# Kernel tuning notes

Measured on AMD Instinct MI355X. Metric: run time of the kernel, lower is better.

## Reference

```python
import jax, jax.numpy as jnp
import numpy as np

V, E, H, C = 100000, 300, 512, 3
SP, SH, B = 64, 32, 128


def lstm_scan(x, Wih, Whh, b):
    # x: [T, B, E]; PyTorch gate order i, f, g, o
    T, Bb, _ = x.shape
    Hh = Whh.shape[1]
    h0 = jnp.zeros((Bb, Hh), x.dtype)

    def step(carry, xt):
        h, c = carry
        g = xt @ Wih.T + h @ Whh.T + b
        i, f, gg, o = jnp.split(g, 4, axis=-1)
        c = jax.nn.sigmoid(f) * c + jax.nn.sigmoid(i) * jnp.tanh(gg)
        h = jax.nn.sigmoid(o) * jnp.tanh(c)
        return (h, c), h

    _, hs = jax.lax.scan(step, (h0, h0), x)
    return hs  # [T, B, H]


def setup_inputs() -> dict:
    key = jax.random.key(0)
    ks = jax.random.split(key, 20)
    inv_sqrt_h = 1.0 / np.sqrt(H).astype(np.float32)

    def u(k, shape, scale):
        return (jax.random.uniform(k, shape, jnp.float32) * 2.0 - 1.0) * scale

    embed_table = jax.random.normal(ks[4], (V, E), jnp.float32) * 0.1
    embed_table = embed_table.at[0].set(0.0)  # padding_idx=0
    return {
        "premise": jax.random.randint(ks[0], (SP, B), 1, V),
        "premise_len": jax.random.randint(ks[1], (B,), 1, SP + 1),
        "hypothesis": jax.random.randint(ks[2], (SH, B), 1, V),
        "hypothesis_len": jax.random.randint(ks[3], (B,), 1, SH + 1),
        "embed_table": embed_table,
        "p_Wih": u(ks[5], (4 * H, E), inv_sqrt_h),
        "p_Whh": u(ks[6], (4 * H, H), inv_sqrt_h),
        "p_b": u(ks[7], (4 * H,), inv_sqrt_h),
        "h_Wih": u(ks[8], (4 * H, E), inv_sqrt_h),
        "h_Whh": u(ks[9], (4 * H, H), inv_sqrt_h),
        "h_b": u(ks[10], (4 * H,), inv_sqrt_h),
        "m_Wih": u(ks[11], (4 * H, 2 * H), inv_sqrt_h),
        "m_Whh": u(ks[12], (4 * H, H), inv_sqrt_h),
        "m_b": u(ks[13], (4 * H,), inv_sqrt_h),
        "w_e": jax.random.uniform(ks[14], (H,), jnp.float32),
        "Ws": u(ks[15], (H, H), np.sqrt(6.0 / (2 * H)).astype(np.float32)),
        "Wt": u(ks[16], (H, H), np.sqrt(6.0 / (2 * H)).astype(np.float32)),
        "Wm": u(ks[17], (H, H), np.sqrt(6.0 / (2 * H)).astype(np.float32)),
        "fc_W": u(ks[18], (C, H), np.sqrt(6.0 / (H + C)).astype(np.float32)),
        "fc_b": jnp.zeros((C,), jnp.float32),
    }


def reference(premise, premise_len, hypothesis, hypothesis_len, embed_table,
              p_Wih, p_Whh, p_b, h_Wih, h_Whh, h_b, m_Wih, m_Whh, m_b,
              w_e, Ws, Wt, Wm, fc_W, fc_b):
    Sp, Bb = premise.shape
    Sh = hypothesis.shape[0]
    Hh = Ws.shape[0]

    # Encoder LSTMs; emulate pack/pad: outputs past length are zeros
    h_s = lstm_scan(embed_table[premise], p_Wih, p_Whh, p_b)  # [Sp,B,H]
    h_s = h_s * (jnp.arange(Sp)[:, None] < premise_len[None, :]).astype(h_s.dtype)[:, :, None]
    h_t = lstm_scan(embed_table[hypothesis], h_Wih, h_Whh, h_b)  # [Sh,B,H]
    h_t = h_t * (jnp.arange(Sh)[:, None] < hypothesis_len[None, :]).astype(h_t.dtype)[:, :, None]

    Ws_hs = jnp.einsum('sbe,he->sbh', h_s, Ws)  # precompute premise projection

    def step(carry, inputs):
        h_m, c_m, h_last = carry
        h_t_k, k = inputs
        q = h_t_k @ Wt.T + h_m @ Wm.T                              # [B,H]
        e = jnp.einsum('sbh,h->sb', jnp.tanh(Ws_hs + q[None]), w_e)  # [Sp,B]
        alpha = jax.nn.softmax(e, axis=0)                           # softmax over premise (no mask, as in original)
        a_k = jnp.einsum('sb,sbh->bh', alpha, h_s)
        m_k = jnp.concatenate([a_k, h_t_k], axis=1)                 # [B,2H]
        g = m_k @ m_Wih.T + h_m @ m_Whh.T + m_b
        i, f, gg, o = jnp.split(g, 4, axis=-1)
        c_new = jax.nn.sigmoid(f) * c_m + jax.nn.sigmoid(i) * jnp.tanh(gg)
        h_new = jax.nn.sigmoid(o) * jnp.tanh(c_new)
        h_last = jnp.where((k + 1 == hypothesis_len)[:, None], h_new, h_last)
        return (h_new, c_new, h_last), None

    z = jnp.zeros((Bb, Hh), h_s.dtype)
    (_, _, h_last), _ = jax.lax.scan(step, (z, z, z), (h_t, jnp.arange(Sh)))
    return h_last @ fc_W.T + fc_b  # [B, C]
```

## Files before the change

### kernel.cpp

```cpp
#include <hip/hip_runtime.h>


#define NWG 256
#define TPB 512

typedef float f8v __attribute__((ext_vector_type(8)));

#define O_XPP      0ull
#define O_HTMW     0ull
#define O_HTWT     8388608ull
#define O_WSHS     10485760ull
#define O_XPH      16777216ull
#define O_HST      25165824ull
#define O_HS2      29360128ull
#define O_HTT      33554432ull
#define O_WIHTP    35651584ull
#define O_WIHTH    36265984ull
#define O_WHHPP    36880384ull
#define O_WHHPH    37928960ull
#define O_DW       38977536ull
#define O_WST      41074688ull
#define O_WTT      41336832ull
#define O_MWIHRT   41598976ull
#define O_BPP      42647552ull
#define O_BPH      42649600ull
#define O_BPM      42651648ull
#define O_HT2      42653696ull
#define O_HMT2     42784768ull
#define O_QBUF     42915840ull
#define O_AK2      42981376ull
#define O_HLAST    43046912ull
#define WS_FLOATS  43112448ull

__device__ unsigned g_cnt = 0u;
__device__ unsigned g_gen = 0u;
__device__ unsigned g_FE[NWG * 16];
__device__ unsigned g_FA[NWG * 16];
__device__ unsigned g_FB[NWG * 16];
__device__ unsigned g_FD[NWG * 16];
__device__ unsigned g_base2 = 0u;

struct Params {
  const int* premise; const int* plen; const int* hyp; const int* hlen;
  const float* embed;
  const float* pWih; const float* pWhh; const float* pb;
  const float* hWih; const float* hWhh; const float* hb;
  const float* mWih; const float* mWhh; const float* mb;
  const float* we; const float* Ws; const float* Wt; const float* Wm;
  const float* fcW; const float* fcb;
  float* out; float* ws;
};

__device__ __forceinline__ float2 sysld2(const float* p){
  unsigned long long u = __hip_atomic_load((const unsigned long long*)p,
      __ATOMIC_RELAXED, __HIP_MEMORY_SCOPE_SYSTEM);
  union { unsigned long long u; float2 f; } c; c.u = u; return c.f;
}
__device__ __forceinline__ void sysst(float* p, float v){
  union { float f; unsigned u; } c; c.f = v;
  __hip_atomic_store((unsigned*)p, c.u, __ATOMIC_RELAXED, __HIP_MEMORY_SCOPE_SYSTEM);
}
__device__ __forceinline__ void fbump(unsigned* a, unsigned v){
  __hip_atomic_store(a, v, __ATOMIC_RELAXED, __HIP_MEMORY_SCOPE_SYSTEM);
}
__device__ __forceinline__ void waitflag(const unsigned* a, unsigned tgt){
  while ((int)(__hip_atomic_load(a, __ATOMIC_RELAXED,
               __HIP_MEMORY_SCOPE_SYSTEM) - tgt) < 0)
    __builtin_amdgcn_s_sleep(1);
}

__device__ __forceinline__ void gbarH(){
  __syncthreads();
  if (threadIdx.x == 0){
    __threadfence();
    unsigned snap = __hip_atomic_load(&g_gen, __ATOMIC_RELAXED, __HIP_MEMORY_SCOPE_AGENT);
    unsigned n = __hip_atomic_fetch_add(&g_cnt, 1u, __ATOMIC_ACQ_REL, __HIP_MEMORY_SCOPE_AGENT);
    if ((n & 255u) == 255u){
      __hip_atomic_store(&g_gen, snap + 1u, __ATOMIC_RELEASE, __HIP_MEMORY_SCOPE_AGENT);
    } else {
      unsigned g;
      do {
        __builtin_amdgcn_s_sleep(2);
        g = __hip_atomic_load(&g_gen, __ATOMIC_ACQUIRE, __HIP_MEMORY_SCOPE_AGENT);
      } while ((int)(g - snap) <= 0);
    }
  }
  __syncthreads();
}

__device__ __forceinline__ float sigf(float x){ return 1.0f/(1.0f + __expf(-x)); }
__device__ __forceinline__ float tanhf_(float x){ return 2.0f/(1.0f + __expf(-2.0f*x)) - 1.0f; }

__device__ __forceinline__ float wsum(float v){
  #pragma unroll
  for (int o = 32; o > 0; o >>= 1) v += __shfl_xor(v, o, 64);
  return v;
}
__device__ __forceinline__ float wmaxr(float v){
  #pragma unroll
  for (int o = 32; o > 0; o >>= 1) v = fmaxf(v, __shfl_xor(v, o, 64));
  return v;
}

__device__ void lstm_enc(int wg, int tid, int lane, int cg, int bg, int T,
    const float* __restrict__ XP, const float* __restrict__ WPair,
    const int* __restrict__ lens, float* hbuf,
    float* __restrict__ houtT, float* __restrict__ hout2, float* lds,
    unsigned tb)
{
  const int b8 = tid & 7, hc32 = (tid >> 3) & 31, gp = tid >> 8;
  const int b = bg*8 + b8, hc = cg*32 + hc32;
  const float* wrow = WPair + (size_t)(hc*2 + gp) * 1024;
  const int mylen = lens[b];
  const int sb = tid >> 6, sk = (tid & 63) * 8;
  float* stage = lds;
  float* xch   = lds + 8*516;
  float c_reg = 0.f;
  const unsigned* peer = &g_FE[(((unsigned)bg << 4) | (lane & 15)) * 16];

  for (int t = 0; t < T; ++t){
    const float* hin  = hbuf + (size_t)(t & 1) * 65536;
    float*       hout = hbuf + (size_t)((t + 1) & 1) * 65536;
    if (lane < 16) waitflag(peer, tb + t);
    if (t > 0){
      const float* src = hin + (size_t)(bg*8 + sb)*512 + sk;
      float2 v0 = sysld2(src), v1 = sysld2(src+2), v2 = sysld2(src+4), v3 = sysld2(src+6);
      float* dst = stage + sb*516 + sk;
      float4 w0 = {v0.x, v0.y, v1.x, v1.y};
      float4 w1 = {v2.x, v2.y, v3.x, v3.y};
      *(float4*)dst = w0; *(float4*)(dst+4) = w1;
    }
    __syncthreads();
    float a0 = 0.f, a1 = 0.f;
    if (t > 0){
      const float* hr = stage + b8*516;
      #pragma unroll 2
      for (int k = 0; k < 512; k += 4){
        float4 h4 = *(const float4*)(hr + k);
        float4 wA = *(const float4*)(wrow + k*2);
        float4 wB = *(const float4*)(wrow + k*2 + 4);
        a0 += h4.x*wA.x + h4.y*wA.z + h4.z*wB.x + h4.w*wB.z;
        a1 += h4.x*wA.y + h4.y*wA.w + h4.z*wB.y + h4.w*wB.w;
      }
    }
    float2 xg = *(const float2*)(XP + ((size_t)t*128 + b)*2048 + hc*4 + gp*2);
    a0 += xg.x; a1 += xg.y;
    if (gp == 1){ xch[(b8*32+hc32)*2+0] = a0; xch[(b8*32+hc32)*2+1] = a1; }
    __syncthreads();
    if (gp == 0){
      float gg = xch[(b8*32+hc32)*2+0], go = xch[(b8*32+hc32)*2+1];
      float iv = sigf(a0), fv = sigf(a1), gv = tanhf_(gg), ov = sigf(go);
      c_reg = fv * c_reg + iv * gv;
      float hv = ov * tanhf_(c_reg);
      sysst(hout + (size_t)b*512 + hc, hv);
      float hm = (t < mylen) ? hv : 0.f;
      houtT[((size_t)t*512 + hc)*128 + b] = hm;
      if (hout2) hout2[((size_t)t*128 + b)*512 + hc] = hm;
    }
    __syncthreads();
    if (tid == 0) fbump(&g_FE[wg*16], tb + t + 1);
  }
}

__global__ __launch_bounds__(TPB, 2) void mlstm(Params p){
  const int wg = blockIdx.x, tid = threadIdx.x;
  const int lane = tid & 63, wave = tid >> 6;
  const int gtid = wg * TPB + tid;
  const int gwave = wg * 8 + wave;
  const int cg = wg & 15, bg = wg >> 4;
  __shared__ float lds[8736];
  __shared__ unsigned sh_base;

  if (tid == 0)
    sh_base = __hip_atomic_load(&g_base2, __ATOMIC_RELAXED, __HIP_MEMORY_SCOPE_SYSTEM);
  __syncthreads();
  const unsigned B = sh_base;

  float* const ws     = p.ws;
  float* const XPp    = ws + O_XPP;
  float* const XPh    = ws + O_XPH;
  float* const htmW   = ws + O_HTMW;
  float* const htWt   = ws + O_HTWT;
  float* const Ws_hs  = ws + O_WSHS;
  float* const h_sT   = ws + O_HST;
  float* const h_s2   = ws + O_HS2;
  float* const h_tT   = ws + O_HTT;
  float* const WihTp  = ws + O_WIHTP;
  float* const WihTh  = ws + O_WIHTH;
  float* const WhhPP  = ws + O_WHHPP;
  float* const WhhPH  = ws + O_WHHPH;
  float* const DW     = ws + O_DW;
  float* const WsT    = ws + O_WST;
  float* const WtT    = ws + O_WTT;
  float* const mWihRT = ws + O_MWIHRT;
  float* const bpP    = ws + O_BPP;
  float* const bpH    = ws + O_BPH;
  float* const bpM    = ws + O_BPM;
  float* const hT2    = ws + O_HT2;
  float* const hmT2   = ws + O_HMT2;
  float* const qbuf   = ws + O_QBUF;
  float* const ak2    = ws + O_AK2;
  float* const hlast  = ws + O_HLAST;

  for (int idx = gtid; idx < 300*2048; idx += NWG*TPB){
    int e = idx >> 11, jp = idx & 2047;
    int oc = (jp & 3) * 512 + (jp >> 2);
    WihTp[idx] = p.pWih[(size_t)oc*300 + e];
    WihTh[idx] = p.hWih[(size_t)oc*300 + e];
  }
  for (int idx = gtid; idx < 1024*512*2; idx += NWG*TPB){
    int g = idx & 1, k = (idx >> 1) & 511, pp = idx >> 10;
    int hc = pp >> 1, gp = pp & 1, oc = (gp*2+g)*512 + hc;
    WhhPP[idx] = p.pWhh[(size_t)oc*512 + k];
    WhhPH[idx] = p.hWhh[(size_t)oc*512 + k];
  }
  for (int idx = gtid; idx < 1024*1024*2; idx += NWG*TPB){
    int g = idx & 1, k = (idx >> 1) & 1023, pp = idx >> 11;
    int hc = pp >> 1, gp = pp & 1, oc = (gp*2+g)*512 + hc;
    DW[idx] = (k < 512) ? p.mWih[(size_t)oc*1024 + k]
                        : p.mWhh[(size_t)oc*512 + (k - 512)];
  }
  for (int idx = gtid; idx < 512*512; idx += NWG*TPB){
    int k = idx >> 9, h = idx & 511;
    WsT[idx] = p.Ws[(size_t)h*512 + k];
    WtT[idx] = p.Wt[(size_t)h*512 + k];
  }
  for (int idx = gtid; idx < 512*2048; idx += NWG*TPB){
    int k = idx >> 11, jp = idx & 2047;
    int oc = (jp & 3) * 512 + (jp >> 2);
    mWihRT[idx] = p.mWih[(size_t)oc*1024 + 512 + k];
  }
  for (int idx = gtid; idx < 2048; idx += NWG*TPB){
    int oc = (idx & 3) * 512 + (idx >> 2);
    bpP[idx] = p.pb[oc]; bpH[idx] = p.hb[oc]; bpM[idx] = p.mb[oc];
  }
  gbarH();

  for (int task = gwave; task < 6144; task += NWG*8){
    const bool prem = task < 4096;
    int rb, cb;
    if (prem){ cb = task >> 10; rb = task & 1023; }
    else { int t2 = task - 4096; cb = t2 >> 9; rb = t2 & 511; }
    const int r0 = rb * 8;
    const int* toks = prem ? p.premise : p.hyp;
    const float* wT = prem ? WihTp : WihTh;
    const float* bias = prem ? bpP : bpH;
    float* outp = prem ? XPp : XPh;
    const int j0 = cb * 512 + lane * 8;
    const float* xr[8];
    #pragma unroll
    for (int r = 0; r < 8; ++r) xr[r] = p.embed + (size_t)toks[r0 + r] * 300;
    f8v bias8 = *(const f8v*)(bias + j0);
    float acc[8][8];
    #pragma unroll
    for (int r = 0; r < 8; ++r){
      #pragma unroll
      for (int i = 0; i < 8; ++i) acc[r][i] = 0.f;
    }
    for (int e = 0; e < 300; ++e){
      f8v w8 = *(const f8v*)(wT + (size_t)e * 2048 + j0);
      #pragma unroll
      for (int r = 0; r < 8; ++r){
        float xv = xr[r][e];
        #pragma unroll
        for (int i = 0; i < 8; ++i) acc[r][i] += xv * w8[i];
      }
    }
    #pragma unroll
    for (int r = 0; r < 8; ++r){
      f8v o8;
      #pragma unroll
      for (int i = 0; i < 8; ++i) o8[i] = acc[r][i] + bias8[i];
      *(f8v*)(outp + (size_t)(r0 + r) * 2048 + j0) = o8;
    }
  }
  gbarH();

  lstm_enc(wg, tid, lane, cg, bg, 64, XPp, WhhPP, p.plen, hT2, h_sT, h_s2, lds, B);
  lstm_enc(wg, tid, lane, cg, bg, 32, XPh, WhhPH, p.hlen, hT2, h_tT, nullptr, lds, B + 64);
  gbarH();

  for (int task = gwave; task < 3584; task += NWG*8){
    const float* src; const float* wT; const float* bias; float* outp;
    int rb, cb, cols;
    if (task < 1024){ rb = task;        cb = 0;            src = h_sT; wT = WsT;    bias = nullptr; outp = Ws_hs; cols = 512; }
    else if (task < 1536){ rb = task-1024; cb = 0;         src = h_tT; wT = WtT;    bias = nullptr; outp = htWt;  cols = 512; }
    else { int t2 = task - 1536; cb = t2 >> 9; rb = t2 & 511; src = h_tT; wT = mWihRT; bias = bpM;  outp = htmW;  cols = 2048; }
    const int r0 = rb * 8;
    const int j0 = cb * 512 + lane * 8;
    const float* xr[8];
    #pragma unroll
    for (int r = 0; r < 8; ++r){
      int row = r0 + r;
      xr[r] = src + (size_t)(row >> 7) * 65536 + (row & 127);
    }
    f8v bias8 = {0,0,0,0,0,0,0,0};
    if (bias) bias8 = *(const f8v*)(bias + j0);
    float acc[8][8];
    #pragma unroll
    for (int r = 0; r < 8; ++r){
      #pragma unroll
      for (int i = 0; i < 8; ++i) acc[r][i] = 0.f;
    }
    for (int k = 0; k < 512; ++k){
      f8v w8 = *(const f8v*)(wT + (size_t)k * cols + j0);
      #pragma unroll
      for (int r = 0; r < 8; ++r){
        float xv = xr[r][(size_t)k * 128];
        #pragma unroll
        for (int i = 0; i < 8; ++i) acc[r][i] += xv * w8[i];
      }
    }
    #pragma unroll
    for (int r = 0; r < 8; ++r){
      f8v o8;
      #pragma unroll
      for (int i = 0; i < 8; ++i) o8[i] = acc[r][i] + bias8[i];
      *(f8v*)(outp + (size_t)(r0 + r) * (size_t)cols + j0) = o8;
    }
  }
  gbarH();

  const int b8 = tid & 7, hc32 = (tid >> 3) & 31, gp = tid >> 8;
  const int mb_ = bg*8 + b8, mhc = cg*32 + hc32;
  const float* dwrow = DW + (size_t)(mhc*2 + gp) * 2048;
  const int hyplen_b = p.hlen[mb_];
  const int sb = tid >> 6, sk = (tid & 63) * 8;
  float* stage  = lds;
  float* xchA   = lds + 8*516;
  float* stage2 = lds;
  float* xch2   = lds + 8*1028;
  float cm_reg = 0.f, hl_reg = 0.f;
  const unsigned* peerFD = &g_FD[(((unsigned)bg << 4) | (lane & 15)) * 16];
  const unsigned* rowFB  = &g_FB[((unsigned)(bg*8) + (lane & 7)) * 16];

  for (int k = 0; k < 32; ++k){
    const float* hmin  = hmT2 + (size_t)(k & 1) * 65536;
    float*       hmout = hmT2 + (size_t)((k + 1) & 1) * 65536;

    if (lane < 16) waitflag(peerFD, B + k);
    else if (lane < 24) waitflag(&g_FB[((unsigned)(bg*8) + (lane - 16)) * 16], B + k);
    if (k > 0){
      const float* src = hmin + (size_t)(bg*8 + sb)*512 + sk;
      float2 v0 = sysld2(src), v1 = sysld2(src+2), v2 = sysld2(src+4), v3 = sysld2(src+6);
      float* dst = stage + sb*516 + sk;
      float4 w0 = {v0.x, v0.y, v1.x, v1.y};
      float4 w1 = {v2.x, v2.y, v3.x, v3.y};
      *(float4*)dst = w0; *(float4*)(dst+4) = w1;
    }
    __syncthreads();
    {
      const int c32 = (tid >> 3) & 31, half = tid >> 8;
      const int c = cg*32 + c32;
      float a = 0.f;
      if (k > 0){
        const float* hr = stage + b8*516 + half*256;
        const float* wr = p.Wm + (size_t)c*512 + half*256;
        #pragma unroll 2
        for (int kk = 0; kk < 256; kk += 4){
          float4 h4 = *(const float4*)(hr + kk);
          float4 w4 = *(const float4*)(wr + kk);
          a += h4.x*w4.x + h4.y*w4.y + h4.z*w4.z + h4.w*w4.w;
        }
      }
      if (half == 1) xchA[c32*8 + b8] = a;
      __syncthreads();
      if (half == 0){
        float v = a + xchA[c32*8 + b8] + htWt[((size_t)k*128 + mb_)*512 + c];
        sysst(qbuf + (size_t)mb_*512 + c, v);
      }
    }
    __syncthreads();
    if (tid == 0) fbump(&g_FA[wg*16], B + k + 1);

    if (wg < 128){
      const int bb = wg;
      if (lane < 16) waitflag(&g_FA[(((unsigned)(bb >> 3) << 4) | lane) * 16], B + k + 1);
      else if (lane < 32) waitflag(&g_FD[(((unsigned)(bb >> 3) << 4) | (lane - 16)) * 16], B + k);
      const float* qb = qbuf + (size_t)bb*512 + lane*8;
      float2 qa = sysld2(qb), qbv = sysld2(qb+2), qc = sysld2(qb+4), qd = sysld2(qb+6);
      float4 q0 = {qa.x, qa.y, qbv.x, qbv.y};
      float4 q1 = {qc.x, qc.y, qd.x, qd.y};
      float4 e0 = *(const float4*)(p.we + lane*8);
      float4 e1 = *(const float4*)(p.we + lane*8 + 4);
      #pragma unroll
      for (int si = 0; si < 8; ++si){
        int s = wave*8 + si;
        const float* wsr = Ws_hs + ((size_t)s*128 + bb)*512 + lane*8;
        float4 s0 = *(const float4*)wsr;
        float4 s1 = *(const float4*)(wsr + 4);
        float v = tanhf_(s0.x + q0.x)*e0.x + tanhf_(s0.y + q0.y)*e0.y
                + tanhf_(s0.z + q0.z)*e0.z + tanhf_(s0.w + q0.w)*e0.w
                + tanhf_(s1.x + q1.x)*e1.x + tanhf_(s1.y + q1.y)*e1.y
                + tanhf_(s1.z + q1.z)*e1.z + tanhf_(s1.w + q1.w)*e1.w;
        v = wsum(v);
        if (lane == 0) lds[s] = v;
      }
      __syncthreads();
      if (wave == 0){
        float v = lds[lane];
        float m = wmaxr(v);
        float ex = __expf(v - m);
        float sm = wsum(ex);
        lds[64 + lane] = ex / sm;
      }
      __syncthreads();
      {
        float acc = 0.f;
        const float* hsb = h_s2 + (size_t)bb*512 + tid;
        #pragma unroll 4
        for (int s = 0; s < 64; s += 4){
          float4 al = *(const float4*)(lds + 64 + s);
          acc += al.x * hsb[(size_t)(s+0)*65536]
               + al.y * hsb[(size_t)(s+1)*65536]
               + al.z * hsb[(size_t)(s+2)*65536]
               + al.w * hsb[(size_t)(s+3)*65536];
        }
        sysst(ak2 + (size_t)bb*512 + tid, acc);
      }
      __syncthreads();
      if (tid == 0) fbump(&g_FB[wg*16], B + k + 1);
    }

    if (lane < 8) waitflag(rowFB, B + k + 1);
    {
      const int sb2 = tid >> 6, c0 = (tid & 63) * 16;
      float* dst = stage2 + sb2*1028 + c0;
      if (c0 < 512){
        const float* src = ak2 + (size_t)(bg*8 + sb2)*512 + c0;
        #pragma unroll
        for (int i = 0; i < 16; i += 4){
          float2 va = sysld2(src + i), vb = sysld2(src + i + 2);
          float4 w = {va.x, va.y, vb.x, vb.y};
          *(float4*)(dst + i) = w;
        }
      } else if (k > 0){
        const float* src = hmin + (size_t)(bg*8 + sb2)*512 + (c0 - 512);
        #pragma unroll
        for (int i = 0; i < 16; i += 4){
          float2 va = sysld2(src + i), vb = sysld2(src + i + 2);
          float4 w = {va.x, va.y, vb.x, vb.y};
          *(float4*)(dst + i) = w;
        }
      } else {
        float4 z = {0.f, 0.f, 0.f, 0.f};
        #pragma unroll
        for (int i = 0; i < 16; i += 4) *(float4*)(dst + i) = z;
      }
    }
    __syncthreads();
    {
      float a0 = 0.f, a1 = 0.f;
      const float* hr = stage2 + b8*1028;
      #pragma unroll 2
      for (int kk = 0; kk < 1024; kk += 4){
        float4 h4 = *(const float4*)(hr + kk);
        float4 wA = *(const float4*)(dwrow + kk*2);
        float4 wB = *(const float4*)(dwrow + kk*2 + 4);
        a0 += h4.x*wA.x + h4.y*wA.z + h4.z*wB.x + h4.w*wB.z;
        a1 += h4.x*wA.y + h4.y*wA.w + h4.z*wB.y + h4.w*wB.w;
      }
      float2 xg = *(const float2*)(htmW + ((size_t)k*128 + mb_)*2048 + mhc*4 + gp*2);
      a0 += xg.x; a1 += xg.y;
      if (gp == 1){ xch2[(b8*32+hc32)*2+0] = a0; xch2[(b8*32+hc32)*2+1] = a1; }
      __syncthreads();
      if (gp == 0){
        float gg = xch2[(b8*32+hc32)*2+0], go = xch2[(b8*32+hc32)*2+1];
        float iv = sigf(a0), fv = sigf(a1), gv = tanhf_(gg), ov = sigf(go);
        cm_reg = fv * cm_reg + iv * gv;
        float hv = ov * tanhf_(cm_reg);
        sysst(hmout + (size_t)mb_*512 + mhc, hv);
        if (k + 1 == hyplen_b) hl_reg = hv;
      }
    }
    __syncthreads();
    if (tid == 0) fbump(&g_FD[wg*16], B + k + 1);
  }

  if (gp == 0) hlast[(size_t)mb_*512 + mhc] = hl_reg;
  gbarH();

  if (tid == 0){
    fbump(&g_FE[wg*16], B + 4096);
    fbump(&g_FA[wg*16], B + 4096);
    fbump(&g_FB[wg*16], B + 4096);
    fbump(&g_FD[wg*16], B + 4096);
    if (wg == 0)
      __hip_atomic_store(&g_base2, B + 4096, __ATOMIC_RELAXED, __HIP_MEMORY_SCOPE_SYSTEM);
  }

  if (wg == 0){
    for (int o = wave; o < 384; o += 8){
      int bb = o / 3, cls = o - bb*3;
      const float* hr = hlast + (size_t)bb*512 + lane*8;
      const float* wr = p.fcW + (size_t)cls*512 + lane*8;
      float4 h0 = *(const float4*)hr, h1 = *(const float4*)(hr + 4);
      float4 w0 = *(const float4*)wr, w1 = *(const float4*)(wr + 4);
      float v = h0.x*w0.x + h0.y*w0.y + h0.z*w0.z + h0.w*w0.w
              + h1.x*w1.x + h1.y*w1.y + h1.z*w1.z + h1.w*w1.w;
      v = wsum(v);
      if (lane == 0) p.out[o] = v + p.fcb[cls];
    }
  }
}

extern "C" void kernel_launch(void* const* d_in, const int* in_sizes, int n_in,
                              void* d_out, int out_size, void* d_ws, size_t ws_size,
                              hipStream_t stream) {
  if (ws_size < WS_FLOATS * sizeof(float)) return;
  Params prm;
  prm.premise = (const int*)d_in[0];
  prm.plen    = (const int*)d_in[1];
  prm.hyp     = (const int*)d_in[2];
  prm.hlen    = (const int*)d_in[3];
  prm.embed   = (const float*)d_in[4];
  prm.pWih    = (const float*)d_in[5];
  prm.pWhh    = (const float*)d_in[6];
  prm.pb      = (const float*)d_in[7];
  prm.hWih    = (const float*)d_in[8];
  prm.hWhh    = (const float*)d_in[9];
  prm.hb      = (const float*)d_in[10];
  prm.mWih    = (const float*)d_in[11];
  prm.mWhh    = (const float*)d_in[12];
  prm.mb      = (const float*)d_in[13];
  prm.we      = (const float*)d_in[14];
  prm.Ws      = (const float*)d_in[15];
  prm.Wt      = (const float*)d_in[16];
  prm.Wm      = (const float*)d_in[17];
  prm.fcW     = (const float*)d_in[18];
  prm.fcb     = (const float*)d_in[19];
  prm.out     = (float*)d_out;
  prm.ws      = (float*)d_ws;
  mlstm<<<dim3(NWG), dim3(TPB), 0, stream>>>(prm);
}
```

Baseline: 4.465 ms.

## Split persistent kernel into staged launches replacing global barriers

The single persistent kernel with software grid barriers is split into six kernel launches: weight repacking, input projections, premise encoder, hypothesis encoder, attention projections and the match LSTM. Launch boundaries now do the work of the grid barriers, and the non-recurrent stages can run with larger grids (1024/768/448 blocks) instead of a fixed 256. Per-step flag bases are read from the per-workgroup flags at kernel start instead of from a shared base counter. This adds launch overhead and changes the flag wait pattern: waits now use thread-index guards followed by __syncthreads, with a longer sleep in the spin loop.

```diff
diff --git a/kernel.cpp b/kernel.cpp
--- a/kernel.cpp
+++ b/kernel.cpp
@@ -32,13 +32,10 @@
 #define O_HLAST    43046912ull
 #define WS_FLOATS  43112448ull
 
-__device__ unsigned g_cnt = 0u;
-__device__ unsigned g_gen = 0u;
 __device__ unsigned g_FE[NWG * 16];
 __device__ unsigned g_FA[NWG * 16];
 __device__ unsigned g_FB[NWG * 16];
 __device__ unsigned g_FD[NWG * 16];
-__device__ unsigned g_base2 = 0u;
 
 struct Params {
   const int* premise; const int* plen; const int* hyp; const int* hlen;
@@ -63,29 +60,11 @@
 __device__ __forceinline__ void fbump(unsigned* a, unsigned v){
   __hip_atomic_store(a, v, __ATOMIC_RELAXED, __HIP_MEMORY_SCOPE_SYSTEM);
 }
+__device__ __forceinline__ unsigned fread_(const unsigned* a){
+  return __hip_atomic_load(a, __ATOMIC_RELAXED, __HIP_MEMORY_SCOPE_SYSTEM);
+}
 __device__ __forceinline__ void waitflag(const unsigned* a, unsigned tgt){
-  while ((int)(__hip_atomic_load(a, __ATOMIC_RELAXED,
-               __HIP_MEMORY_SCOPE_SYSTEM) - tgt) < 0)
-    __builtin_amdgcn_s_sleep(1);
-}
-
-__device__ __forceinline__ void gbarH(){
-  __syncthreads();
-  if (threadIdx.x == 0){
-    __threadfence();
-    unsigned snap = __hip_atomic_load(&g_gen, __ATOMIC_RELAXED, __HIP_MEMORY_SCOPE_AGENT);
-    unsigned n = __hip_atomic_fetch_add(&g_cnt, 1u, __ATOMIC_ACQ_REL, __HIP_MEMORY_SCOPE_AGENT);
-    if ((n & 255u) == 255u){
-      __hip_atomic_store(&g_gen, snap + 1u, __ATOMIC_RELEASE, __HIP_MEMORY_SCOPE_AGENT);
-    } else {
-      unsigned g;
-      do {
-        __builtin_amdgcn_s_sleep(2);
-        g = __hip_atomic_load(&g_gen, __ATOMIC_ACQUIRE, __HIP_MEMORY_SCOPE_AGENT);
-      } while ((int)(g - snap) <= 0);
-    }
-  }
-  __syncthreads();
+  while ((int)(fread_(a) - tgt) < 0) __builtin_amdgcn_s_sleep(2);
 }
 
 __device__ __forceinline__ float sigf(float x){ return 1.0f/(1.0f + __expf(-x)); }
@@ -102,89 +81,10 @@
   return v;
 }
 
-__device__ void lstm_enc(int wg, int tid, int lane, int cg, int bg, int T,
-    const float* __restrict__ XP, const float* __restrict__ WPair,
-    const int* __restrict__ lens, float* hbuf,
-    float* __restrict__ houtT, float* __restrict__ hout2, float* lds,
-    unsigned tb)
-{
-  const int b8 = tid & 7, hc32 = (tid >> 3) & 31, gp = tid >> 8;
-  const int b = bg*8 + b8, hc = cg*32 + hc32;
-  const float* wrow = WPair + (size_t)(hc*2 + gp) * 1024;
-  const int mylen = lens[b];
-  const int sb = tid >> 6, sk = (tid & 63) * 8;
-  float* stage = lds;
-  float* xch   = lds + 8*516;
-  float c_reg = 0.f;
-  const unsigned* peer = &g_FE[(((unsigned)bg << 4) | (lane & 15)) * 16];
-
-  for (int t = 0; t < T; ++t){
-    const float* hin  = hbuf + (size_t)(t & 1) * 65536;
-    float*       hout = hbuf + (size_t)((t + 1) & 1) * 65536;
-    if (lane < 16) waitflag(peer, tb + t);
-    if (t > 0){
-      const float* src = hin + (size_t)(bg*8 + sb)*512 + sk;
-      float2 v0 = sysld2(src), v1 = sysld2(src+2), v2 = sysld2(src+4), v3 = sysld2(src+6);
-      float* dst = stage + sb*516 + sk;
-      float4 w0 = {v0.x, v0.y, v1.x, v1.y};
-      float4 w1 = {v2.x, v2.y, v3.x, v3.y};
-      *(float4*)dst = w0; *(float4*)(dst+4) = w1;
-    }
-    __syncthreads();
-    float a0 = 0.f, a1 = 0.f;
-    if (t > 0){
-      const float* hr = stage + b8*516;
-      #pragma unroll 2
-      for (int k = 0; k < 512; k += 4){
-        float4 h4 = *(const float4*)(hr + k);
-        float4 wA = *(const float4*)(wrow + k*2);
-        float4 wB = *(const float4*)(wrow + k*2 + 4);
-        a0 += h4.x*wA.x + h4.y*wA.z + h4.z*wB.x + h4.w*wB.z;
-        a1 += h4.x*wA.y + h4.y*wA.w + h4.z*wB.y + h4.w*wB.w;
-      }
-    }
-    float2 xg = *(const float2*)(XP + ((size_t)t*128 + b)*2048 + hc*4 + gp*2);
-    a0 += xg.x; a1 += xg.y;
-    if (gp == 1){ xch[(b8*32+hc32)*2+0] = a0; xch[(b8*32+hc32)*2+1] = a1; }
-    __syncthreads();
-    if (gp == 0){
-      float gg = xch[(b8*32+hc32)*2+0], go = xch[(b8*32+hc32)*2+1];
-      float iv = sigf(a0), fv = sigf(a1), gv = tanhf_(gg), ov = sigf(go);
-      c_reg = fv * c_reg + iv * gv;
-      float hv = ov * tanhf_(c_reg);
-      sysst(hout + (size_t)b*512 + hc, hv);
-      float hm = (t < mylen) ? hv : 0.f;
-      houtT[((size_t)t*512 + hc)*128 + b] = hm;
-      if (hout2) hout2[((size_t)t*128 + b)*512 + hc] = hm;
-    }
-    __syncthreads();
-    if (tid == 0) fbump(&g_FE[wg*16], tb + t + 1);
-  }
-}
-
-__global__ __launch_bounds__(TPB, 2) void mlstm(Params p){
-  const int wg = blockIdx.x, tid = threadIdx.x;
-  const int lane = tid & 63, wave = tid >> 6;
-  const int gtid = wg * TPB + tid;
-  const int gwave = wg * 8 + wave;
-  const int cg = wg & 15, bg = wg >> 4;
-  __shared__ float lds[8736];
-  __shared__ unsigned sh_base;
-
-  if (tid == 0)
-    sh_base = __hip_atomic_load(&g_base2, __ATOMIC_RELAXED, __HIP_MEMORY_SCOPE_SYSTEM);
-  __syncthreads();
-  const unsigned B = sh_base;
-
-  float* const ws     = p.ws;
-  float* const XPp    = ws + O_XPP;
-  float* const XPh    = ws + O_XPH;
-  float* const htmW   = ws + O_HTMW;
-  float* const htWt   = ws + O_HTWT;
-  float* const Ws_hs  = ws + O_WSHS;
-  float* const h_sT   = ws + O_HST;
-  float* const h_s2   = ws + O_HS2;
-  float* const h_tT   = ws + O_HTT;
+__global__ __launch_bounds__(TPB) void k_s0(Params p){
+  const int tid0 = blockIdx.x * TPB + threadIdx.x;
+  const int stride = gridDim.x * TPB;
+  float* const ws = p.ws;
   float* const WihTp  = ws + O_WIHTP;
   float* const WihTh  = ws + O_WIHTH;
   float* const WhhPP  = ws + O_WHHPP;
@@ -196,47 +96,54 @@
   float* const bpP    = ws + O_BPP;
   float* const bpH    = ws + O_BPH;
   float* const bpM    = ws + O_BPM;
-  float* const hT2    = ws + O_HT2;
-  float* const hmT2   = ws + O_HMT2;
-  float* const qbuf   = ws + O_QBUF;
-  float* const ak2    = ws + O_AK2;
-  float* const hlast  = ws + O_HLAST;
-
-  for (int idx = gtid; idx < 300*2048; idx += NWG*TPB){
+
+  for (int idx = tid0; idx < 300*2048; idx += stride){
     int e = idx >> 11, jp = idx & 2047;
     int oc = (jp & 3) * 512 + (jp >> 2);
     WihTp[idx] = p.pWih[(size_t)oc*300 + e];
     WihTh[idx] = p.hWih[(size_t)oc*300 + e];
   }
-  for (int idx = gtid; idx < 1024*512*2; idx += NWG*TPB){
+  for (int idx = tid0; idx < 1024*512*2; idx += stride){
     int g = idx & 1, k = (idx >> 1) & 511, pp = idx >> 10;
     int hc = pp >> 1, gp = pp & 1, oc = (gp*2+g)*512 + hc;
     WhhPP[idx] = p.pWhh[(size_t)oc*512 + k];
     WhhPH[idx] = p.hWhh[(size_t)oc*512 + k];
   }
-  for (int idx = gtid; idx < 1024*1024*2; idx += NWG*TPB){
+  for (int idx = tid0; idx < 1024*1024*2; idx += stride){
     int g = idx & 1, k = (idx >> 1) & 1023, pp = idx >> 11;
     int hc = pp >> 1, gp = pp & 1, oc = (gp*2+g)*512 + hc;
     DW[idx] = (k < 512) ? p.mWih[(size_t)oc*1024 + k]
                         : p.mWhh[(size_t)oc*512 + (k - 512)];
   }
-  for (int idx = gtid; idx < 512*512; idx += NWG*TPB){
+  for (int idx = tid0; idx < 512*512; idx += stride){
     int k = idx >> 9, h = idx & 511;
     WsT[idx] = p.Ws[(size_t)h*512 + k];
     WtT[idx] = p.Wt[(size_t)h*512 + k];
   }
-  for (int idx = gtid; idx < 512*2048; idx += NWG*TPB){
+  for (int idx = tid0; idx < 512*2048; idx += stride){
     int k = idx >> 11, jp = idx & 2047;
     int oc = (jp & 3) * 512 + (jp >> 2);
     mWihRT[idx] = p.mWih[(size_t)oc*1024 + 512 + k];
   }
-  for (int idx = gtid; idx < 2048; idx += NWG*TPB){
+  for (int idx = tid0; idx < 2048; idx += stride){
     int oc = (idx & 3) * 512 + (idx >> 2);
     bpP[idx] = p.pb[oc]; bpH[idx] = p.hb[oc]; bpM[idx] = p.mb[oc];
   }
-  gbarH();
-
-  for (int task = gwave; task < 6144; task += NWG*8){
+}
+
+__global__ __launch_bounds__(TPB) void k_s1(Params p){
+  const int tid = threadIdx.x, lane = tid & 63, wave = tid >> 6;
+  const int gwave = blockIdx.x * 8 + wave;
+  const int wstride = gridDim.x * 8;
+  float* const ws = p.ws;
+  float* const XPp   = ws + O_XPP;
+  float* const XPh   = ws + O_XPH;
+  const float* WihTp = ws + O_WIHTP;
+  const float* WihTh = ws + O_WIHTH;
+  const float* bpP   = ws + O_BPP;
+  const float* bpH   = ws + O_BPH;
+
+  for (int task = gwave; task < 6144; task += wstride){
     const bool prem = task < 4096;
     int rb, cb;
     if (prem){ cb = task >> 10; rb = task & 1023; }
@@ -274,13 +181,105 @@
       *(f8v*)(outp + (size_t)(r0 + r) * 2048 + j0) = o8;
     }
   }
-  gbarH();
-
-  lstm_enc(wg, tid, lane, cg, bg, 64, XPp, WhhPP, p.plen, hT2, h_sT, h_s2, lds, B);
-  lstm_enc(wg, tid, lane, cg, bg, 32, XPh, WhhPH, p.hlen, hT2, h_tT, nullptr, lds, B + 64);
-  gbarH();
-
-  for (int task = gwave; task < 3584; task += NWG*8){
+}
+
+__device__ void lstm_enc(int wg, int tid, int cg, int bg, int T,
+    const float* __restrict__ XP, const float* __restrict__ WPair,
+    const int* __restrict__ lens, float* hbuf,
+    float* __restrict__ houtT, float* __restrict__ hout2, float* lds,
+    unsigned B)
+{
+  const int b8 = tid & 7, hc32 = (tid >> 3) & 31, gp = tid >> 8;
+  const int b = bg*8 + b8, hc = cg*32 + hc32;
+  const float* wrow = WPair + (size_t)(hc*2 + gp) * 1024;
+  const int mylen = lens[b];
+  const int sb = tid >> 6, sk = (tid & 63) * 8;
+  float* stage = lds;
+  float* xch   = lds + 8*516;
+  float c_reg = 0.f;
+
+  for (int t = 0; t < T; ++t){
+    const float* hin  = hbuf + (size_t)(t & 1) * 65536;
+    float*       hout = hbuf + (size_t)((t + 1) & 1) * 65536;
+    if (t > 0){
+      if (tid < 16) waitflag(&g_FE[(unsigned)(bg*16 + tid)*16], B + t);
+      __syncthreads();
+      const float* src = hin + (size_t)(bg*8 + sb)*512 + sk;
+      float2 v0 = sysld2(src), v1 = sysld2(src+2), v2 = sysld2(src+4), v3 = sysld2(src+6);
+      float* dst = stage + sb*516 + sk;
+      float4 w0 = {v0.x, v0.y, v1.x, v1.y};
+      float4 w1 = {v2.x, v2.y, v3.x, v3.y};
+      *(float4*)dst = w0; *(float4*)(dst+4) = w1;
+    }
+    __syncthreads();
+    float a0 = 0.f, a1 = 0.f;
+    if (t > 0){
+      const float* hr = stage + b8*516;
+      #pragma unroll 2
+      for (int k = 0; k < 512; k += 4){
+        float4 h4 = *(const float4*)(hr + k);
+        float4 wA = *(const float4*)(wrow + k*2);
+        float4 wB = *(const float4*)(wrow + k*2 + 4);
+        a0 += h4.x*wA.x + h4.y*wA.z + h4.z*wB.x + h4.w*wB.z;
+        a1 += h4.x*wA.y + h4.y*wA.w + h4.z*wB.y + h4.w*wB.w;
+      }
+    }
+    float2 xg = *(const float2*)(XP + ((size_t)t*128 + b)*2048 + hc*4 + gp*2);
+    a0 += xg.x; a1 += xg.y;
+    if (gp == 1){ xch[(b8*32+hc32)*2+0] = a0; xch[(b8*32+hc32)*2+1] = a1; }
+    __syncthreads();
+    if (gp == 0){
+      float gg = xch[(b8*32+hc32)*2+0], go = xch[(b8*32+hc32)*2+1];
+      float iv = sigf(a0), fv = sigf(a1), gv = tanhf_(gg), ov = sigf(go);
+      c_reg = fv * c_reg + iv * gv;
+      float hv = ov * tanhf_(c_reg);
+      sysst(hout + (size_t)b*512 + hc, hv);
+      float hm = (t < mylen) ? hv : 0.f;
+      houtT[((size_t)t*512 + hc)*128 + b] = hm;
+      if (hout2) hout2[((size_t)t*128 + b)*512 + hc] = hm;
+    }
+    __syncthreads();
+    if (tid == 0) fbump(&g_FE[wg*16], B + t + 1);
+  }
+}
+
+__global__ __launch_bounds__(TPB, 2) void k_encp(Params p){
+  const int wg = blockIdx.x, tid = threadIdx.x;
+  const int cg = wg & 15, bg = wg >> 4;
+  __shared__ float lds[4640];
+  __shared__ unsigned shB;
+  if (tid == 0) shB = fread_(&g_FE[wg*16]);
+  __syncthreads();
+  lstm_enc(wg, tid, cg, bg, 64, p.ws + O_XPP, p.ws + O_WHHPP, p.plen,
+           p.ws + O_HT2, p.ws + O_HST, p.ws + O_HS2, lds, shB);
+}
+__global__ __launch_bounds__(TPB, 2) void k_ench(Params p){
+  const int wg = blockIdx.x, tid = threadIdx.x;
+  const int cg = wg & 15, bg = wg >> 4;
+  __shared__ float lds[4640];
+  __shared__ unsigned shB;
+  if (tid == 0) shB = fread_(&g_FE[wg*16]);
+  __syncthreads();
+  lstm_enc(wg, tid, cg, bg, 32, p.ws + O_XPH, p.ws + O_WHHPH, p.hlen,
+           p.ws + O_HT2, p.ws + O_HTT, nullptr, lds, shB);
+}
+
+__global__ __launch_bounds__(TPB) void k_s4(Params p){
+  const int tid = threadIdx.x, lane = tid & 63, wave = tid >> 6;
+  const int gwave = blockIdx.x * 8 + wave;
+  const int wstride = gridDim.x * 8;
+  float* const ws = p.ws;
+  const float* h_sT   = ws + O_HST;
+  const float* h_tT   = ws + O_HTT;
+  const float* WsT    = ws + O_WST;
+  const float* WtT    = ws + O_WTT;
+  const float* mWihRT = ws + O_MWIHRT;
+  const float* bpM    = ws + O_BPM;
+  float* const Ws_hs  = ws + O_WSHS;
+  float* const htWt   = ws + O_HTWT;
+  float* const htmW   = ws + O_HTMW;
+
+  for (int task = gwave; task < 3584; task += wstride){
     const float* src; const float* wT; const float* bias; float* outp;
     int rb, cb, cols;
     if (task < 1024){ rb = task;        cb = 0;            src = h_sT; wT = WsT;    bias = nullptr; outp = Ws_hs; cols = 512; }
@@ -319,7 +318,28 @@
       *(f8v*)(outp + (size_t)(r0 + r) * (size_t)cols + j0) = o8;
     }
   }
-  gbarH();
+}
+
+__global__ __launch_bounds__(TPB, 2) void k_match(Params p){
+  const int wg = blockIdx.x, tid = threadIdx.x;
+  const int lane = tid & 63, wave = tid >> 6;
+  const int cg = wg & 15, bg = wg >> 4;
+  __shared__ float lds[8736];
+  __shared__ unsigned shB;
+  if (tid == 0) shB = fread_(&g_FD[wg*16]);
+  __syncthreads();
+  const unsigned B = shB;
+
+  float* const ws = p.ws;
+  const float* htmW  = ws + O_HTMW;
+  const float* htWt  = ws + O_HTWT;
+  const float* Ws_hs = ws + O_WSHS;
+  const float* h_s2  = ws + O_HS2;
+  const float* DW    = ws + O_DW;
+  float* const hmT2  = ws + O_HMT2;
+  float* const qbuf  = ws + O_QBUF;
+  float* const ak2   = ws + O_AK2;
+  float* const hlast = ws + O_HLAST;
 
   const int b8 = tid & 7, hc32 = (tid >> 3) & 31, gp = tid >> 8;
   const int mb_ = bg*8 + b8, mhc = cg*32 + hc32;
@@ -331,15 +351,14 @@
   float* stage2 = lds;
   float* xch2   = lds + 8*1028;
   float cm_reg = 0.f, hl_reg = 0.f;
-  const unsigned* peerFD = &g_FD[(((unsigned)bg << 4) | (lane & 15)) * 16];
-  const unsigned* rowFB  = &g_FB[((unsigned)(bg*8) + (lane & 7)) * 16];
 
   for (int k = 0; k < 32; ++k){
     const float* hmin  = hmT2 + (size_t)(k & 1) * 65536;
     float*       hmout = hmT2 + (size_t)((k + 1) & 1) * 65536;
 
-    if (lane < 16) waitflag(peerFD, B + k);
-    else if (lane < 24) waitflag(&g_FB[((unsigned)(bg*8) + (lane - 16)) * 16], B + k);
+    if (tid < 16) waitflag(&g_FD[(unsigned)(bg*16 + tid)*16], B + k);
+    else if (tid < 24) waitflag(&g_FB[(unsigned)(bg*8 + tid - 16)*16], B + k);
+    __syncthreads();
     if (k > 0){
       const float* src = hmin + (size_t)(bg*8 + sb)*512 + sk;
       float2 v0 = sysld2(src), v1 = sysld2(src+2), v2 = sysld2(src+4), v3 = sysld2(src+6);
@@ -375,8 +394,9 @@
 
     if (wg < 128){
       const int bb = wg;
-      if (lane < 16) waitflag(&g_FA[(((unsigned)(bb >> 3) << 4) | lane) * 16], B + k + 1);
-      else if (lane < 32) waitflag(&g_FD[(((unsigned)(bb >> 3) << 4) | (lane - 16)) * 16], B + k);
+      if (tid < 16) waitflag(&g_FA[(unsigned)((bb >> 3)*16 + tid)*16], B + k + 1);
+      else if (tid < 32) waitflag(&g_FD[(unsigned)((bb >> 3)*16 + tid - 16)*16], B + k);
+      __syncthreads();
       const float* qb = qbuf + (size_t)bb*512 + lane*8;
       float2 qa = sysld2(qb), qbv = sysld2(qb+2), qc = sysld2(qb+4), qd = sysld2(qb+6);
       float4 q0 = {qa.x, qa.y, qbv.x, qbv.y};
@@ -422,7 +442,8 @@
       if (tid == 0) fbump(&g_FB[wg*16], B + k + 1);
     }
 
-    if (lane < 8) waitflag(rowFB, B + k + 1);
+    if (tid < 8) waitflag(&g_FB[(unsigned)(bg*8 + tid)*16], B + k + 1);
+    __syncthreads();
     {
       const int sb2 = tid >> 6, c0 = (tid & 63) * 16;
       float* dst = stage2 + sb2*1028 + c0;
@@ -477,27 +498,25 @@
     if (tid == 0) fbump(&g_FD[wg*16], B + k + 1);
   }
 
-  if (gp == 0) hlast[(size_t)mb_*512 + mhc] = hl_reg;
-  gbarH();
-
+  if (gp == 0) sysst(hlast + (size_t)mb_*512 + mhc, hl_reg);
+  __syncthreads();
   if (tid == 0){
-    fbump(&g_FE[wg*16], B + 4096);
-    fbump(&g_FA[wg*16], B + 4096);
-    fbump(&g_FB[wg*16], B + 4096);
-    fbump(&g_FD[wg*16], B + 4096);
-    if (wg == 0)
-      __hip_atomic_store(&g_base2, B + 4096, __ATOMIC_RELAXED, __HIP_MEMORY_SCOPE_SYSTEM);
+    fbump(&g_FD[wg*16], B + 40);
+    fbump(&g_FA[wg*16], B + 40);
+    fbump(&g_FB[wg*16], B + 40);
   }
 
   if (wg == 0){
+    if (tid < NWG) waitflag(&g_FD[(unsigned)tid*16], B + 40);
+    __syncthreads();
     for (int o = wave; o < 384; o += 8){
       int bb = o / 3, cls = o - bb*3;
       const float* hr = hlast + (size_t)bb*512 + lane*8;
       const float* wr = p.fcW + (size_t)cls*512 + lane*8;
-      float4 h0 = *(const float4*)hr, h1 = *(const float4*)(hr + 4);
+      float2 ha = sysld2(hr), hb = sysld2(hr+2), hc2 = sysld2(hr+4), hd = sysld2(hr+6);
       float4 w0 = *(const float4*)wr, w1 = *(const float4*)(wr + 4);
-      float v = h0.x*w0.x + h0.y*w0.y + h0.z*w0.z + h0.w*w0.w
-              + h1.x*w1.x + h1.y*w1.y + h1.z*w1.z + h1.w*w1.w;
+      float v = ha.x*w0.x + ha.y*w0.y + hb.x*w0.z + hb.y*w0.w
+              + hc2.x*w1.x + hc2.y*w1.y + hd.x*w1.z + hd.y*w1.w;
       v = wsum(v);
       if (lane == 0) p.out[o] = v + p.fcb[cls];
     }
@@ -531,5 +550,11 @@
   prm.fcb     = (const float*)d_in[19];
   prm.out     = (float*)d_out;
   prm.ws      = (float*)d_ws;
-  mlstm<<<dim3(NWG), dim3(TPB), 0, stream>>>(prm);
-}
+
+  k_s0   <<<dim3(1024), dim3(TPB), 0, stream>>>(prm);
+  k_s1   <<<dim3(768),  dim3(TPB), 0, stream>>>(prm);
+  k_encp <<<dim3(NWG),  dim3(TPB), 0, stream>>>(prm);
+  k_ench <<<dim3(NWG),  dim3(TPB), 0, stream>>>(prm);
+  k_s4   <<<dim3(448),  dim3(TPB), 0, stream>>>(prm);
+  k_match<<<dim3(NWG),  dim3(TPB), 0, stream>>>(prm);
+}
```

After: 4.305 ms. 3.6% less time.
